# Performance work log

Measured on AMD Instinct MI355X. Metric: run time of the kernel, lower is better.

The kernel has to match this reference:

```python
import math
import jax, jax.numpy as jnp
import numpy as np

B, T, D = 16, 512, 64  # N = B*T = 8192


def setup_inputs() -> dict:
    key = jax.random.key(0)
    k1, k2, k3, k4 = jax.random.split(key, 4)
    z_seq = jax.random.normal(k1, (B, T, D), dtype=jnp.float32)
    prior_mean = jax.random.normal(k2, (D,), dtype=jnp.float32) * 0.1
    prior_std = jax.random.uniform(k3, (D,), dtype=jnp.float32, minval=0.5, maxval=1.5)
    z_prior = jax.random.normal(k4, (B * T, D), dtype=jnp.float32)
    return {"z_seq": z_seq, "prior_mean": prior_mean, "prior_std": prior_std, "z_prior": z_prior}


def _sq_dists(x, y):
    # squared euclidean distances, [n, m]; clamp tiny negatives from cancellation
    xx = jnp.sum(x * x, axis=-1)
    yy = jnp.sum(y * y, axis=-1)
    d2 = xx[:, None] + yy[None, :] - 2.0 * (x @ y.T)
    return jnp.maximum(d2, 0.0)


def _rbf(x, y, sigma):
    return jnp.exp(-_sq_dists(x, y) / (2.0 * sigma * sigma))


def reference(z_seq, prior_mean, prior_std, z_prior):
    d = z_seq.shape[-1]
    sigma = math.sqrt(d)
    z = z_seq.reshape(-1, d)                      # [N, d]
    z_norm = (z - prior_mean) / prior_std          # [N, d]
    x, y = z_norm, z_prior
    n, m = x.shape[0], y.shape[0]
    kxx = _rbf(x, x, sigma)
    kyy = _rbf(y, y, sigma)
    kxy = _rbf(x, y, sigma)
    mmd = ((kxx.sum() - jnp.trace(kxx)) / (n * (n - 1))
           + (kyy.sum() - jnp.trace(kyy)) / (m * (m - 1))
           - 2.0 * kxy.mean())
    return jnp.maximum(mmd, 0.0)
```

## Files before the change

kernel.cpp:

```cpp
#include <hip/hip_runtime.h>
#include <hip/hip_bf16.h>
#include <math.h>


using short8  = __attribute__((ext_vector_type(8))) short;
using f32x4   = __attribute__((ext_vector_type(4))) float;
using float4v = __attribute__((ext_vector_type(4))) float;

#define NROWS 8192
#define DDIM  64
#define GRID_MAIN (1024 + 2 * 544)

#define PRESCALE 0.15014030109830622f

__device__ __forceinline__ float exp2_fast(float x) {
#if __has_builtin(__builtin_amdgcn_exp2f)
    return __builtin_amdgcn_exp2f(x);
#else
    return exp2f(x);
#endif
}

__global__ __launch_bounds__(256) void mmd_prep(
    const float* __restrict__ z_seq, const float* __restrict__ pmean,
    const float* __restrict__ pstd, const float* __restrict__ z_prior,
    __hip_bfloat16* __restrict__ Xb, __hip_bfloat16* __restrict__ Yb,
    float* __restrict__ sxx, float* __restrict__ syy)
{
    const int tid  = threadIdx.x;
    const int lane = tid & 63;
    const int wid  = tid >> 6;
    const int w    = blockIdx.x * 4 + wid;
    const int sub  = lane >> 4;
    const int row  = w * 4 + sub;
    const int d0   = (lane & 15) * 4;

    float4v v;
    __hip_bfloat16* dst;
    float* sdst;
    int r;
    if (row < NROWS) {
        r = row;
        float4v z  = *reinterpret_cast<const float4v*>(z_seq + (size_t)r * DDIM + d0);
        float4v pm = *reinterpret_cast<const float4v*>(pmean + d0);
        float4v ps = *reinterpret_cast<const float4v*>(pstd + d0);
#pragma unroll
        for (int k = 0; k < 4; ++k) v[k] = (z[k] - pm[k]) / ps[k];
        dst = Xb; sdst = sxx;
    } else {
        r = row - NROWS;
        v = *reinterpret_cast<const float4v*>(z_prior + (size_t)r * DDIM + d0);
        dst = Yb; sdst = syy;
    }

    ushort4 hb;
    float sq = 0.0f;
#pragma unroll
    for (int k = 0; k < 4; ++k) {
        __hip_bfloat16 b = __float2bfloat16(v[k] * PRESCALE);
        reinterpret_cast<__hip_bfloat16*>(&hb)[k] = b;
        float vb = __bfloat162float(b);
        sq += vb * vb;
    }
    *reinterpret_cast<ushort4*>(dst + (size_t)r * DDIM + d0) = hb;

#pragma unroll
    for (int off = 8; off; off >>= 1) sq += __shfl_xor(sq, off, 64);
    if ((lane & 15) == 0) sdst[r] = 0.5f * sq;
}

__global__ __launch_bounds__(256) void mmd_main(
    const __hip_bfloat16* __restrict__ Xb, const __hip_bfloat16* __restrict__ Yb,
    const float* __restrict__ sxx, const float* __restrict__ syy,
    double* __restrict__ partials)
{
    __shared__ __align__(16) char Bs[16384];

    const int bid = blockIdx.x;

    int bi, bj;
    bool sym;
    const __hip_bfloat16* A;
    const __hip_bfloat16* Bp;
    const float* sa;
    const float* sb;

    if (bid < 1024) {
        sym = false;
        bi = bid >> 6; bj = bid & 63;
        A = Xb; Bp = Yb; sa = sxx; sb = syy;
    } else {
        sym = true;
        const int t = bid - 1024;
        const int u = t >> 1;
        int g = (int)((sqrtf((float)(2 * u + 1)) - 1.0f) * 0.5f);
        while (2 * (g + 1) * (g + 2) <= u) ++g;
        while (2 * g * (g + 1) > u) --g;
        const int rem = u - 2 * g * (g + 1);
        const int q   = rem / (g + 1);
        bj = 4 * g + q;
        bi = rem - q * (g + 1);
        if (t & 1) { A = Yb; Bp = Yb; sa = syy; sb = syy; }
        else       { A = Xb; Bp = Xb; sa = sxx; sb = sxx; }
    }

    const int tid  = threadIdx.x;
    const int lane = tid & 63;
    const int wid  = tid >> 6;
    const int quad = lane >> 4;
    const int l15  = lane & 15;

    const int iBlock = bi * 512;
    const int jBlock = bj * 128;

    {
        const char* gB = (const char*)Bp + (size_t)jBlock * 128;
#pragma unroll
        for (int k = 0; k < 4; ++k) {
            const int c  = wid * 4 + k;
            const int x  = c * 1024 + lane * 16;
            const int gx = x ^ (((x >> 7) & 7) << 4);
            __builtin_amdgcn_global_load_lds(
                (const __attribute__((address_space(1))) void*)(gB + gx),
                (__attribute__((address_space(3))) void*)(Bs + c * 1024),
                16, 0, 0);
        }
    }

    int i0 = iBlock + wid * 32;

    short8 af[2][2];
    f32x4  nsx[2];
#pragma unroll
    for (int mt = 0; mt < 2; ++mt) {
        const int ar = i0 + mt * 16 + l15;
#pragma unroll
        for (int ks = 0; ks < 2; ++ks)
            af[mt][ks] = *reinterpret_cast<const short8*>(
                A + (size_t)ar * DDIM + ks * 32 + quad * 8);
        f32x4 s4 = *reinterpret_cast<const f32x4*>(sa + i0 + mt * 16 + quad * 4);
        nsx[mt] = -s4;
    }

    float nsy[8];
#pragma unroll
    for (int nt = 0; nt < 8; ++nt) nsy[nt] = -sb[jBlock + l15 + nt * 16];

    __syncthreads();

    const int swz   = (l15 & 7) << 4;
    const int off0  = (quad * 16) ^ swz;
    const int off1  = (quad * 16 + 64) ^ swz;
    const char* lb0 = Bs + l15 * 128;

    float ls0 = 0.0f, ls1 = 0.0f, ls2 = 0.0f, ls3 = 0.0f;

    for (int c = 0; c < 4; ++c) {
#pragma unroll
        for (int nt = 0; nt < 8; ++nt) {
            const int jt = jBlock + nt * 16;
            if (sym && jt < i0) continue;

            const char* lp = lb0 + nt * 16 * 128;
            short8 b0 = *reinterpret_cast<const short8*>(lp + off0);
            short8 b1 = *reinterpret_cast<const short8*>(lp + off1);

#pragma unroll
            for (int mt = 0; mt < 2; ++mt) {
                const int it = i0 + mt * 16;
                if (sym && jt < it) continue;

                f32x4 acc4;
#pragma unroll
                for (int r = 0; r < 4; ++r) acc4[r] = nsx[mt][r] + nsy[nt];
                acc4 = __builtin_amdgcn_mfma_f32_16x16x32_bf16(af[mt][0], b0, acc4, 0, 0, 0);
                acc4 = __builtin_amdgcn_mfma_f32_16x16x32_bf16(af[mt][1], b1, acc4, 0, 0, 0);

                if (sym && jt == it) {
                    ls0 += (l15 > quad * 4 + 0) ? exp2_fast(acc4[0]) : 0.0f;
                    ls1 += (l15 > quad * 4 + 1) ? exp2_fast(acc4[1]) : 0.0f;
                    ls2 += (l15 > quad * 4 + 2) ? exp2_fast(acc4[2]) : 0.0f;
                    ls3 += (l15 > quad * 4 + 3) ? exp2_fast(acc4[3]) : 0.0f;
                } else {
                    ls0 += exp2_fast(acc4[0]);
                    ls1 += exp2_fast(acc4[1]);
                    ls2 += exp2_fast(acc4[2]);
                    ls3 += exp2_fast(acc4[3]);
                }
            }
        }

        if (c < 3) {
            const int i0n = i0 + 128;
            if (sym && jBlock + 112 < i0n) break;
#pragma unroll
            for (int mt = 0; mt < 2; ++mt) {
                const int ar = i0n + mt * 16 + l15;
#pragma unroll
                for (int ks = 0; ks < 2; ++ks)
                    af[mt][ks] = *reinterpret_cast<const short8*>(
                        A + (size_t)ar * DDIM + ks * 32 + quad * 8);
                f32x4 s4 = *reinterpret_cast<const f32x4*>(sa + i0n + mt * 16 + quad * 4);
                nsx[mt] = -s4;
            }
            i0 = i0n;
        }
    }

    float lsum = (ls0 + ls1) + (ls2 + ls3);

#pragma unroll
    for (int off = 32; off; off >>= 1) lsum += __shfl_xor(lsum, off, 64);

    __shared__ float ws4[4];
    if (lane == 0) ws4[wid] = lsum;
    __syncthreads();
    if (tid == 0) {
        double tot = (double)ws4[0] + (double)ws4[1] + (double)ws4[2] + (double)ws4[3];
        partials[bid] = tot;
    }
}

__global__ __launch_bounds__(256) void mmd_final(
    const double* __restrict__ partials, float* __restrict__ out)
{
    const int tid = threadIdx.x;
    const double cs = 2.0 / (8192.0 * 8191.0);
    const double cx = -2.0 / (8192.0 * 8192.0);

    double s = 0.0;
    for (int idx = tid; idx < GRID_MAIN; idx += 256) {
        double c = (idx < 1024) ? cx : cs;
        s += partials[idx] * c;
    }
#pragma unroll
    for (int off = 32; off; off >>= 1) s += __shfl_xor(s, off, 64);

    __shared__ double wsum[4];
    const int lane = tid & 63, wid = tid >> 6;
    if (lane == 0) wsum[wid] = s;
    __syncthreads();
    if (tid == 0) {
        double mmd = wsum[0] + wsum[1] + wsum[2] + wsum[3];
        out[0] = (float)(mmd > 0.0 ? mmd : 0.0);
    }
}

extern "C" void kernel_launch(void* const* d_in, const int* in_sizes, int n_in,
                              void* d_out, int out_size, void* d_ws, size_t ws_size,
                              hipStream_t stream) {
    const float* z_seq   = (const float*)d_in[0];
    const float* pmean   = (const float*)d_in[1];
    const float* pstd    = (const float*)d_in[2];
    const float* z_prior = (const float*)d_in[3];
    float* out = (float*)d_out;

    char* ws = (char*)d_ws;
    __hip_bfloat16* Xb = (__hip_bfloat16*)(ws);
    __hip_bfloat16* Yb = (__hip_bfloat16*)(ws + (1u << 20));
    float* sxx = (float*)(ws + (2u << 20));
    float* syy = (float*)(ws + (2u << 20) + 32768);
    double* partials = (double*)(ws + (2u << 20) + 65536);

    mmd_prep<<<dim3(1024), dim3(256), 0, stream>>>(
        z_seq, pmean, pstd, z_prior, Xb, Yb, sxx, syy);
    mmd_main<<<dim3(GRID_MAIN), dim3(256), 0, stream>>>(
        Xb, Yb, sxx, syy, partials);
    mmd_final<<<dim3(1), dim3(256), 0, stream>>>(partials, out);
}
```

Measured before the change: 100.8 us.

## Switch to 32x32x16 MFMA tiles and factor column norm out of exponent

```diff
diff --git a/kernel.cpp b/kernel.cpp
--- a/kernel.cpp
+++ b/kernel.cpp
@@ -5,6 +5,7 @@
 
 using short8  = __attribute__((ext_vector_type(8))) short;
 using f32x4   = __attribute__((ext_vector_type(4))) float;
+using f32x16  = __attribute__((ext_vector_type(16))) float;
 using float4v = __attribute__((ext_vector_type(4))) float;
 
 #define NROWS 8192
@@ -66,7 +67,7 @@
 
 #pragma unroll
     for (int off = 8; off; off >>= 1) sq += __shfl_xor(sq, off, 64);
-    if ((lane & 15) == 0) sdst[r] = 0.5f * sq;
+    if ((lane & 15) == 0) sdst[r] = -0.5f * sq;
 }
 
 __global__ __launch_bounds__(256) void mmd_main(
@@ -107,8 +108,8 @@
     const int tid  = threadIdx.x;
     const int lane = tid & 63;
     const int wid  = tid >> 6;
-    const int quad = lane >> 4;
-    const int l15  = lane & 15;
+    const int l31  = lane & 31;
+    const int h    = lane >> 5;
 
     const int iBlock = bi * 512;
     const int jBlock = bj * 128;
@@ -129,79 +130,95 @@
 
     int i0 = iBlock + wid * 32;
 
-    short8 af[2][2];
-    f32x4  nsx[2];
-#pragma unroll
-    for (int mt = 0; mt < 2; ++mt) {
-        const int ar = i0 + mt * 16 + l15;
-#pragma unroll
-        for (int ks = 0; ks < 2; ++ks)
-            af[mt][ks] = *reinterpret_cast<const short8*>(
-                A + (size_t)ar * DDIM + ks * 32 + quad * 8);
-        f32x4 s4 = *reinterpret_cast<const f32x4*>(sa + i0 + mt * 16 + quad * 4);
-        nsx[mt] = -s4;
-    }
-
-    float nsy[8];
-#pragma unroll
-    for (int nt = 0; nt < 8; ++nt) nsy[nt] = -sb[jBlock + l15 + nt * 16];
+    short8 af0, af1, af2, af3;
+    f32x16 cin;
+    {
+        const char* arow = (const char*)A + (size_t)(i0 + l31) * 128 + 16 * h;
+        af0 = *reinterpret_cast<const short8*>(arow);
+        af1 = *reinterpret_cast<const short8*>(arow + 32);
+        af2 = *reinterpret_cast<const short8*>(arow + 64);
+        af3 = *reinterpret_cast<const short8*>(arow + 96);
+        const float* sna = sa + i0 + 4 * h;
+#pragma unroll
+        for (int q = 0; q < 4; ++q) {
+            f32x4 t = *reinterpret_cast<const f32x4*>(sna + 8 * q);
+            cin[4 * q + 0] = t[0]; cin[4 * q + 1] = t[1];
+            cin[4 * q + 2] = t[2]; cin[4 * q + 3] = t[3];
+        }
+    }
+
+    float nsy4[4];
+#pragma unroll
+    for (int nt = 0; nt < 4; ++nt) nsy4[nt] = sb[jBlock + nt * 32 + l31];
 
     __syncthreads();
 
-    const int swz   = (l15 & 7) << 4;
-    const int off0  = (quad * 16) ^ swz;
-    const int off1  = (quad * 16 + 64) ^ swz;
-    const char* lb0 = Bs + l15 * 128;
+    const int swz = (l31 & 7) << 4;
+    const int bo0 = (16 * h +  0) ^ swz;
+    const int bo1 = (16 * h + 32) ^ swz;
+    const int bo2 = (16 * h + 64) ^ swz;
+    const int bo3 = (16 * h + 96) ^ swz;
+    const char* lbbase = Bs + l31 * 128;
 
     float ls0 = 0.0f, ls1 = 0.0f, ls2 = 0.0f, ls3 = 0.0f;
 
     for (int c = 0; c < 4; ++c) {
 #pragma unroll
-        for (int nt = 0; nt < 8; ++nt) {
-            const int jt = jBlock + nt * 16;
+        for (int nt = 0; nt < 4; ++nt) {
+            const int jt = jBlock + nt * 32;
             if (sym && jt < i0) continue;
 
-            const char* lp = lb0 + nt * 16 * 128;
-            short8 b0 = *reinterpret_cast<const short8*>(lp + off0);
-            short8 b1 = *reinterpret_cast<const short8*>(lp + off1);
-
-#pragma unroll
-            for (int mt = 0; mt < 2; ++mt) {
-                const int it = i0 + mt * 16;
-                if (sym && jt < it) continue;
-
-                f32x4 acc4;
-#pragma unroll
-                for (int r = 0; r < 4; ++r) acc4[r] = nsx[mt][r] + nsy[nt];
-                acc4 = __builtin_amdgcn_mfma_f32_16x16x32_bf16(af[mt][0], b0, acc4, 0, 0, 0);
-                acc4 = __builtin_amdgcn_mfma_f32_16x16x32_bf16(af[mt][1], b1, acc4, 0, 0, 0);
-
-                if (sym && jt == it) {
-                    ls0 += (l15 > quad * 4 + 0) ? exp2_fast(acc4[0]) : 0.0f;
-                    ls1 += (l15 > quad * 4 + 1) ? exp2_fast(acc4[1]) : 0.0f;
-                    ls2 += (l15 > quad * 4 + 2) ? exp2_fast(acc4[2]) : 0.0f;
-                    ls3 += (l15 > quad * 4 + 3) ? exp2_fast(acc4[3]) : 0.0f;
-                } else {
-                    ls0 += exp2_fast(acc4[0]);
-                    ls1 += exp2_fast(acc4[1]);
-                    ls2 += exp2_fast(acc4[2]);
-                    ls3 += exp2_fast(acc4[3]);
+            const char* lp = lbbase + nt * 4096;
+            short8 b0 = *reinterpret_cast<const short8*>(lp + bo0);
+            short8 b1 = *reinterpret_cast<const short8*>(lp + bo1);
+            short8 b2 = *reinterpret_cast<const short8*>(lp + bo2);
+            short8 b3 = *reinterpret_cast<const short8*>(lp + bo3);
+
+            f32x16 acc = __builtin_amdgcn_mfma_f32_32x32x16_bf16(af0, b0, cin, 0, 0, 0);
+            acc = __builtin_amdgcn_mfma_f32_32x32x16_bf16(af1, b1, acc, 0, 0, 0);
+            acc = __builtin_amdgcn_mfma_f32_32x32x16_bf16(af2, b2, acc, 0, 0, 0);
+            acc = __builtin_amdgcn_mfma_f32_32x32x16_bf16(af3, b3, acc, 0, 0, 0);
+
+            const float ey = exp2_fast(nsy4[nt]);
+
+            if (sym && jt == i0) {
+                const int rb = 4 * h;
+#pragma unroll
+                for (int r = 0; r < 16; ++r) {
+                    const int rowr = rb + (r & 3) + 8 * (r >> 2);
+                    float v = exp2_fast(acc[r]) * ey;
+                    float m = (l31 > rowr) ? v : 0.0f;
+                    if ((r & 3) == 0) ls0 += m;
+                    else if ((r & 3) == 1) ls1 += m;
+                    else if ((r & 3) == 2) ls2 += m;
+                    else ls3 += m;
+                }
+            } else {
+#pragma unroll
+                for (int r = 0; r < 16; ++r) {
+                    float e = exp2_fast(acc[r]);
+                    if ((r & 3) == 0) ls0 = fmaf(e, ey, ls0);
+                    else if ((r & 3) == 1) ls1 = fmaf(e, ey, ls1);
+                    else if ((r & 3) == 2) ls2 = fmaf(e, ey, ls2);
+                    else ls3 = fmaf(e, ey, ls3);
                 }
             }
         }
 
         if (c < 3) {
             const int i0n = i0 + 128;
-            if (sym && jBlock + 112 < i0n) break;
-#pragma unroll
-            for (int mt = 0; mt < 2; ++mt) {
-                const int ar = i0n + mt * 16 + l15;
-#pragma unroll
-                for (int ks = 0; ks < 2; ++ks)
-                    af[mt][ks] = *reinterpret_cast<const short8*>(
-                        A + (size_t)ar * DDIM + ks * 32 + quad * 8);
-                f32x4 s4 = *reinterpret_cast<const f32x4*>(sa + i0n + mt * 16 + quad * 4);
-                nsx[mt] = -s4;
+            if (sym && jBlock + 96 < i0n) break;
+            const char* arow = (const char*)A + (size_t)(i0n + l31) * 128 + 16 * h;
+            af0 = *reinterpret_cast<const short8*>(arow);
+            af1 = *reinterpret_cast<const short8*>(arow + 32);
+            af2 = *reinterpret_cast<const short8*>(arow + 64);
+            af3 = *reinterpret_cast<const short8*>(arow + 96);
+            const float* sna = sa + i0n + 4 * h;
+#pragma unroll
+            for (int q = 0; q < 4; ++q) {
+                f32x4 t = *reinterpret_cast<const f32x4*>(sna + 8 * q);
+                cin[4 * q + 0] = t[0]; cin[4 * q + 1] = t[1];
+                cin[4 * q + 2] = t[2]; cin[4 * q + 3] = t[3];
             }
             i0 = i0n;
         }
```

Measured after the change: 95.79 us. 5.0% less time.
